# Optimization experiments

Hardware: AMD Instinct MI355X
Metric: run time of the kernel (lower is better)

The kernel has to match this reference:

```python
import jax, jax.numpy as jnp
import numpy as np

B, T = 8, 1024
IN_FEAT = 1024
N_FEAT = 1024
N_HEAD = 16
D_K = N_FEAT // N_HEAD
KERNEL = 11
LEFT_PAD = (KERNEL - 1) // 2  # sanm_shift=0
RIGHT_PAD = KERNEL - 1 - LEFT_PAD


def setup_inputs() -> dict:
    key = jax.random.key(0)
    ks = jax.random.split(key, 7)
    hidden_states = jax.random.normal(ks[0], (B, T, IN_FEAT), dtype=jnp.float32)
    mask = jax.random.randint(ks[1], (B, 1, T), 0, 2, dtype=jnp.int32)
    s_qkv = 1.0 / np.sqrt(IN_FEAT)
    s_out = 1.0 / np.sqrt(N_FEAT)
    W_qkv = jax.random.normal(ks[2], (3 * N_FEAT, IN_FEAT), dtype=jnp.float32) * s_qkv
    b_qkv = jnp.zeros((3 * N_FEAT,), dtype=jnp.float32)
    W_out = jax.random.normal(ks[3], (N_FEAT, N_FEAT), dtype=jnp.float32) * s_out
    b_out = jnp.zeros((N_FEAT,), dtype=jnp.float32)
    fsmn_kernel = jax.random.normal(ks[4], (N_FEAT, 1, KERNEL), dtype=jnp.float32) * (1.0 / KERNEL)
    return {"hidden_states": hidden_states, "mask": mask, "W_qkv": W_qkv,
            "b_qkv": b_qkv, "W_out": W_out, "b_out": b_out, "fsmn_kernel": fsmn_kernel}


def _fsmn(v, maskf, fsmn_kernel):
    # v: [B,T,D], maskf: [B,T,1]
    vm = v * maskf
    x = jnp.transpose(vm, (0, 2, 1))  # [B,D,T]
    x = jnp.pad(x, ((0, 0), (0, 0), (LEFT_PAD, RIGHT_PAD)))
    # depthwise conv1d (cross-correlation, matching torch Conv1d)
    y = jax.lax.conv_general_dilated(
        x, fsmn_kernel, window_strides=(1,), padding='VALID',
        dimension_numbers=('NCH', 'OIH', 'NCH'), feature_group_count=N_FEAT)
    y = jnp.transpose(y, (0, 2, 1)) + vm  # [B,T,D]
    return y * maskf


def reference(hidden_states, mask, W_qkv, b_qkv, W_out, b_out, fsmn_kernel):
    b, t, _ = hidden_states.shape
    qkv = jnp.einsum('btf,of->bto', hidden_states, W_qkv) + b_qkv  # [B,T,3*N_FEAT]
    q, k, v = jnp.split(qkv, 3, axis=-1)
    def heads(x):
        return jnp.transpose(x.reshape(b, t, N_HEAD, D_K), (0, 2, 1, 3))  # [B,H,T,D_K]
    q_h, k_h, v_h = heads(q), heads(k), heads(v)

    maskf = mask.reshape(b, t, 1).astype(hidden_states.dtype)
    fsmn_memory = _fsmn(v, maskf, fsmn_kernel)

    scale = D_K ** -0.5
    scores = jnp.einsum('bhqd,bhkd->bhqk', q_h * scale, k_h)  # [B,H,T,T]
    mask_keys = (mask.reshape(b, 1, 1, t) == 0)  # True where padded
    scores = jnp.where(mask_keys, -jnp.inf, scores)
    attn = jax.nn.softmax(scores, axis=-1)
    attn = jnp.where(mask_keys, 0.0, attn)
    ctx = jnp.einsum('bhqk,bhkd->bhqd', attn, v_h)  # [B,H,T,D_K]
    ctx = jnp.transpose(ctx, (0, 2, 1, 3)).reshape(b, t, N_FEAT)
    att_outs = jnp.einsum('btf,of->bto', ctx, W_out) + b_out
    return att_outs + fsmn_memory
```

## Files before the change

### kernel.cpp

```cpp
#include <hip/hip_runtime.h>
#include <stdint.h>


typedef uint16_t u16;
typedef float f32x4 __attribute__((ext_vector_type(4)));
typedef __bf16 bf16x8 __attribute__((ext_vector_type(8)));
typedef __bf16 bf16x2 __attribute__((ext_vector_type(2)));
typedef u16 u16x8 __attribute__((ext_vector_type(8)));
typedef u16 u16x4 __attribute__((ext_vector_type(4)));
typedef short s16x4 __attribute__((ext_vector_type(4)));

__device__ __forceinline__ u16 f2bf(float f) {
    union { float f; uint32_t u; } c; c.f = f;
    uint32_t u = c.u;
    return (u16)((u + 0x7fffu + ((u >> 16) & 1u)) >> 16);
}
__device__ __forceinline__ float bf2f(u16 h) {
    union { uint32_t u; float f; } c; c.u = ((uint32_t)h) << 16;
    return c.f;
}
__device__ __forceinline__ uint32_t pack_bf16(float a, float b) {
    bf16x2 t; t[0] = (__bf16)a; t[1] = (__bf16)b;
    union { bf16x2 v; uint32_t u; } c; c.v = t; return c.u;
}

__global__ __launch_bounds__(256) void cvt_f32_bf16(const float* __restrict__ src,
                                                    u16* __restrict__ dst, int n) {
    int i = (blockIdx.x * 256 + threadIdx.x) * 4;
    if (i >= n) return;
    float4 v = *reinterpret_cast<const float4*>(src + i);
    ushort4 o;
    o.x = f2bf(v.x); o.y = f2bf(v.y); o.z = f2bf(v.z); o.w = f2bf(v.w);
    *reinterpret_cast<ushort4*>(dst + i) = o;
}

__global__ void maskbits_kernel(const int* __restrict__ mask, uint32_t* __restrict__ mb) {
    int i = threadIdx.x;
    int b = i >> 5, c = i & 31;
    uint32_t u = 0;
    for (int j = 0; j < 32; ++j)
        u |= (mask[(b << 10) + c * 32 + j] ? 1u : 0u) << j;
    mb[i] = u;
}

__global__ __launch_bounds__(256) void fsmn_kt(const float* __restrict__ fk,
                                               float* __restrict__ kt) {
    int idx = blockIdx.x * 256 + threadIdx.x;
    if (idx < 11 * 1024) {
        int j = idx >> 10, c = idx & 1023;
        kt[idx] = fk[c * 11 + j];
    }
}

__global__ __launch_bounds__(256) void transpose_v(const u16* __restrict__ vn,
                                                   u16* __restrict__ vt) {
    __shared__ u16 ts[64][68];
    const int tid = threadIdx.x;
    const int bh = blockIdx.x >> 4;
    const int kc = blockIdx.x & 15;
    const u16* src = vn + ((size_t)bh << 16) + (size_t)kc * 64 * 64;
#pragma unroll
    for (int it = 0; it < 2; ++it) {
        int ch = it * 256 + tid;
        int k = ch >> 3, g = ch & 7;
        *reinterpret_cast<u16x8*>(&ts[k][g * 8]) =
            *reinterpret_cast<const u16x8*>(src + k * 64 + g * 8);
    }
    __syncthreads();
    u16* dst = vt + ((size_t)bh << 16) + kc * 64;
#pragma unroll
    for (int it = 0; it < 2; ++it) {
        int ch = it * 256 + tid;
        int d = ch >> 3, gk = ch & 7;
        u16x8 v;
#pragma unroll
        for (int j = 0; j < 8; ++j) v[j] = ts[gk * 8 + j][d];
        *reinterpret_cast<u16x8*>(dst + (size_t)d * 1024 + gk * 8) = v;
    }
}

template<int MODE>
__global__ __launch_bounds__(512, 4) void gemm_bk32(
    const u16* __restrict__ A, const u16* __restrict__ Bw, int M, int N, int K,
    int ntiles_n, const float* __restrict__ bias,
    u16* __restrict__ qo, u16* __restrict__ ko, u16* __restrict__ vo,
    float* __restrict__ out)
{
    __shared__ u16 lds[24576];
    const int t = threadIdx.x;
    const int lane = t & 63;
    const int wave = t >> 6;
    const int wr = wave >> 2, wc = wave & 3;
    const int lr = lane & 15, lq = lane >> 4;
    const int r3 = lane >> 2, c4 = lane & 3;
    const int cpx = gridDim.x >> 3;
    const int bid = (blockIdx.x & 7) * cpx + (blockIdx.x >> 3);
    const int m0 = (bid / ntiles_n) * 128;
    const int n0 = (bid % ntiles_n) * 256;
    const int NT = K >> 5;

    const u16* AgW  = A  + (size_t)(m0 + wave * 16 + r3) * K + c4 * 8;
    const u16* BgW0 = Bw + (size_t)(n0 + wave * 16 + r3) * K + c4 * 8;
    const u16* BgW1 = BgW0 + (size_t)128 * K;

    auto stage = [&](int buf, int tile) {
        u16* dA  = lds + buf * 12288 + wave * 512;
        u16* dB0 = lds + buf * 12288 + 4096 + wave * 512;
        u16* dB1 = dB0 + 4096;
        __builtin_amdgcn_global_load_lds(
            (const __attribute__((address_space(1))) void*)(AgW + tile * 32),
            (__attribute__((address_space(3))) void*)dA, 16, 0, 0);
        __builtin_amdgcn_global_load_lds(
            (const __attribute__((address_space(1))) void*)(BgW0 + tile * 32),
            (__attribute__((address_space(3))) void*)dB0, 16, 0, 0);
        __builtin_amdgcn_global_load_lds(
            (const __attribute__((address_space(1))) void*)(BgW1 + tile * 32),
            (__attribute__((address_space(3))) void*)dB1, 16, 0, 0);
    };

    f32x4 acc[4][4];
#pragma unroll
    for (int i = 0; i < 4; ++i)
#pragma unroll
        for (int j = 0; j < 4; ++j) acc[i][j] = (f32x4){0.f, 0.f, 0.f, 0.f};

    stage(0, 0);
    asm volatile("s_waitcnt vmcnt(0)" ::: "memory");
    __builtin_amdgcn_s_barrier();

    for (int T = 0; T < NT; ++T) {
        const int p = T & 1;
        const u16* Ab = lds + p * 12288;
        const u16* Bb = Ab + 4096;
        bf16x8 a[4], bb[4];
#pragma unroll
        for (int mm = 0; mm < 4; ++mm)
            a[mm] = *reinterpret_cast<const bf16x8*>(Ab + (wr * 64 + mm * 16 + lr) * 32 + lq * 8);
#pragma unroll
        for (int nn = 0; nn < 4; ++nn)
            bb[nn] = *reinterpret_cast<const bf16x8*>(Bb + (wc * 64 + nn * 16 + lr) * 32 + lq * 8);
        if (T + 1 < NT) stage(p ^ 1, T + 1);
        __builtin_amdgcn_s_setprio(1);
#pragma unroll
        for (int mm = 0; mm < 4; ++mm)
#pragma unroll
            for (int nn = 0; nn < 4; ++nn)
                acc[mm][nn] = __builtin_amdgcn_mfma_f32_16x16x32_bf16(a[mm], bb[nn], acc[mm][nn], 0, 0, 0);
        __builtin_amdgcn_s_setprio(0);
        if (T + 1 < NT) asm volatile("s_waitcnt vmcnt(0)" ::: "memory");
        __builtin_amdgcn_s_barrier();
    }

#pragma unroll
    for (int m = 0; m < 4; ++m) {
        int row = m0 + wr * 64 + m * 16 + lq * 4;
#pragma unroll
        for (int n = 0; n < 4; ++n) {
            int col = n0 + wc * 64 + n * 16 + lr;
            float bv = bias[col];
#pragma unroll
            for (int r = 0; r < 4; ++r) {
                float val = acc[m][n][r] + bv;
                int rr = row + r;
                if (MODE == 0) {
                    int part = col >> 10;
                    int cc = col & 1023;
                    int h = cc >> 6, d = cc & 63;
                    int b = rr >> 10, tt = rr & 1023;
                    size_t bh = (size_t)(b * 16 + h);
                    u16* dst = (part == 0) ? qo : (part == 1) ? ko : vo;
                    dst[((bh << 10) + tt) * 64 + d] = f2bf(part == 0 ? val * 0.18033688011f : val);
                } else {
                    size_t o = (size_t)rr * N + col;
                    out[o] += val;
                }
            }
        }
    }
}

__global__ __launch_bounds__(256) void fsmn_v3(const u16* __restrict__ vt,
                                               const int* __restrict__ mask,
                                               const float* __restrict__ kt,
                                               float* __restrict__ out)
{
    __shared__ float vs[64][147];
    __shared__ float ms[144];
    const int tid = threadIdx.x;
    const int tc = blockIdx.x & 7;
    const int bh = blockIdx.x >> 3;
    const int b = bh >> 4, h = bh & 15;
    const int t0 = tc * 128;
    const u16* vrow = vt + ((size_t)bh << 16);
    const int* mrow = mask + (b << 10);

    if (tid < 144) {
        int tt = t0 - 8 + tid;
        ms[tid] = (tt >= 0 && tt < 1024) ? (float)mrow[tt] : 0.f;
    }
    const int sd = tid >> 2;
    const int ci0 = tid & 3;
#pragma unroll
    for (int it = 0; it < 5; ++it) {
        int ci = ci0 + it * 4;
        if (ci < 18) {
            int tbase = t0 - 8 + ci * 8;
            if (tbase >= 0 && tbase < 1024) {
                u16x8 v8 = *reinterpret_cast<const u16x8*>(vrow + (size_t)sd * 1024 + tbase);
#pragma unroll
                for (int j = 0; j < 8; ++j)
                    vs[sd][ci * 8 + j] = bf2f((u16)v8[j]) * (float)mrow[tbase + j];
            } else {
#pragma unroll
                for (int j = 0; j < 8; ++j) vs[sd][ci * 8 + j] = 0.f;
            }
        }
    }
    __syncthreads();

    const int dd = tid & 63;
    const int tg = tid >> 6;
    const int c = h * 64 + dd;
    float kc[11];
#pragma unroll
    for (int j = 0; j < 11; ++j) kc[j] = kt[j * 1024 + c];

    const int tl0 = tg * 32;
    float w[11];
#pragma unroll
    for (int j = 0; j < 11; ++j) w[j] = vs[dd][3 + tl0 + j];
    float* orow = out + ((size_t)(b * 1024 + t0 + tl0)) * 1024 + c;
#pragma unroll 4
    for (int s = 0; s < 32; ++s) {
        float acc = 0.f;
#pragma unroll
        for (int j = 0; j < 11; ++j) acc += kc[j] * w[j];
        float mf = ms[8 + tl0 + s];
        orow[(size_t)s * 1024] = (acc + w[5]) * mf;
#pragma unroll
        for (int j = 0; j < 10; ++j) w[j] = w[j + 1];
        w[10] = vs[dd][3 + tl0 + s + 11];
    }
}

__global__ __launch_bounds__(512) void attn_v9(const u16* __restrict__ qg,
                                               const u16* __restrict__ kg,
                                               const u16* __restrict__ vtg,
                                               const uint32_t* __restrict__ mbits,
                                               u16* __restrict__ ctx)
{
    __shared__ u16 K_s[2][64 * 64];
    __shared__ u16 V_s[2][64 * 64];
    const int t = threadIdx.x;
    const int lane = t & 63;
    const int w = t >> 6;
    const int lr = lane & 15, lq = lane >> 4;
    const int bh = blockIdx.x & 127;
    const int qc = blockIdx.x >> 7;
    const int b = bh >> 4, h = bh & 15;
    const size_t base = (size_t)bh << 16;
    const u16* kb = kg + base;
    const u16* vb = vtg + base;
    const int q0 = qc * 256 + w * 32;

    bf16x8 qf[2][2];
#pragma unroll
    for (int qt = 0; qt < 2; ++qt)
#pragma unroll
        for (int kk = 0; kk < 2; ++kk)
            qf[qt][kk] = *reinterpret_cast<const bf16x8*>(
                qg + base + (size_t)(q0 + qt * 16 + lr) * 64 + kk * 32 + lq * 8);

    f32x4 oacc[2][4];
    f32x4 oacc_l[2];
#pragma unroll
    for (int qt = 0; qt < 2; ++qt) {
        oacc_l[qt] = (f32x4){0.f, 0.f, 0.f, 0.f};
#pragma unroll
        for (int dt = 0; dt < 4; ++dt) oacc[qt][dt] = (f32x4){0.f, 0.f, 0.f, 0.f};
    }

    s16x4 ones_f;
#pragma unroll
    for (int j = 0; j < 4; ++j) ones_f[j] = (short)0x3F80;

    const uint32_t* mrow = mbits + b * 32;

    auto stage = [&](int bufi, int tile) {
        const int k0s = tile * 64;
        int ch = w * 64 + lane;
        int row = ch >> 3, c7 = ch & 7;
        int sc = (c7 ^ (row & 7)) * 8;
        const u16* srcK = kb + (size_t)(k0s + row) * 64 + sc;
        const u16* srcV = vb + (size_t)row * 1024 + k0s + sc;
        u16* dK = &K_s[bufi][(size_t)(w * 64) * 8];
        u16* dV = &V_s[bufi][(size_t)(w * 64) * 8];
        __builtin_amdgcn_global_load_lds(
            (const __attribute__((address_space(1))) void*)srcK,
            (__attribute__((address_space(3))) void*)dK, 16, 0, 0);
        __builtin_amdgcn_global_load_lds(
            (const __attribute__((address_space(1))) void*)srcV,
            (__attribute__((address_space(3))) void*)dV, 16, 0, 0);
    };

    int cur = 0;
    stage(0, 0);
    asm volatile("s_waitcnt vmcnt(0)");
    __syncthreads();

    for (int it = 0; it < 16; ++it) {
        if (it < 15) stage(cur ^ 1, it + 1);

        const u16* Kb = K_s[cur];
        bf16x8 kf[4][2];
#pragma unroll
        for (int kt = 0; kt < 4; ++kt) {
            int row = kt * 16 + lr;
#pragma unroll
            for (int kk = 0; kk < 2; ++kk) {
                int g = (kk * 4 + lq) ^ (row & 7);
                kf[kt][kk] = *reinterpret_cast<const bf16x8*>(Kb + row * 64 + g * 8);
            }
        }

        const uint32_t mw0 = mrow[it * 2], mw1 = mrow[it * 2 + 1];
        uint32_t mb_[4];
        mb_[0] = mw0 >> (lq * 4);
        mb_[1] = mw0 >> (16 + lq * 4);
        mb_[2] = mw1 >> (lq * 4);
        mb_[3] = mw1 >> (16 + lq * 4);
        f32x4 ma[4];
#pragma unroll
        for (int kt = 0; kt < 4; ++kt)
#pragma unroll
            for (int r = 0; r < 4; ++r)
                ma[kt][r] = (mb_[kt] & (1u << r)) ? 0.f : -3e38f;

        const u16* Vb = V_s[cur];
        s16x4 vf[4][4];
#pragma unroll
        for (int ks = 0; ks < 4; ++ks)
#pragma unroll
            for (int dt = 0; dt < 4; ++dt) {
                int row = dt * 16 + lr;
                int g = (ks * 2 + (lq >> 1)) ^ (row & 7);
                vf[ks][dt] = *reinterpret_cast<const s16x4*>(Vb + row * 64 + g * 8 + (lq & 1) * 4);
            }

#pragma unroll
        for (int qt = 0; qt < 2; ++qt) {
            f32x4 s[4];
            __builtin_amdgcn_s_setprio(1);
#pragma unroll
            for (int kt = 0; kt < 4; ++kt) {
                s[kt] = __builtin_amdgcn_mfma_f32_16x16x32_bf16(kf[kt][0], qf[qt][0], ma[kt], 0, 0, 0);
                s[kt] = __builtin_amdgcn_mfma_f32_16x16x32_bf16(kf[kt][1], qf[qt][1], s[kt], 0, 0, 0);
            }
            __builtin_amdgcn_s_setprio(0);

            union { uint32_t u[2]; s16x4 v; } pa[4];
#pragma unroll
            for (int kt = 0; kt < 4; ++kt) {
                float p0 = __builtin_amdgcn_exp2f(s[kt][0]);
                float p1 = __builtin_amdgcn_exp2f(s[kt][1]);
                float p2 = __builtin_amdgcn_exp2f(s[kt][2]);
                float p3 = __builtin_amdgcn_exp2f(s[kt][3]);
                pa[kt].u[0] = pack_bf16(p0, p1);
                pa[kt].u[1] = pack_bf16(p2, p3);
            }

            __builtin_amdgcn_s_setprio(1);
#pragma unroll
            for (int dt = 0; dt < 4; ++dt) {
                f32x4 o = oacc[qt][dt];
#pragma unroll
                for (int kt = 0; kt < 4; ++kt)
                    o = __builtin_amdgcn_mfma_f32_16x16x16bf16_1k(vf[kt][dt], pa[kt].v, o, 0, 0, 0);
                oacc[qt][dt] = o;
            }
#pragma unroll
            for (int kt = 0; kt < 4; ++kt)
                oacc_l[qt] = __builtin_amdgcn_mfma_f32_16x16x16bf16_1k(ones_f, pa[kt].v, oacc_l[qt], 0, 0, 0);
            __builtin_amdgcn_s_setprio(0);
        }

        asm volatile("s_waitcnt vmcnt(0)" ::: "memory");
        __syncthreads();
        cur ^= 1;
    }

#pragma unroll
    for (int qt = 0; qt < 2; ++qt) {
        float li = 1.f / oacc_l[qt][0];
        int trow = q0 + qt * 16 + lr;
        u16* crow = ctx + ((size_t)(b << 10) + trow) * 1024 + h * 64;
#pragma unroll
        for (int dt = 0; dt < 4; ++dt) {
            f32x4 o = oacc[qt][dt];
            u16x4 pkv;
            pkv[0] = f2bf(o[0] * li); pkv[1] = f2bf(o[1] * li);
            pkv[2] = f2bf(o[2] * li); pkv[3] = f2bf(o[3] * li);
            *reinterpret_cast<u16x4*>(crow + dt * 16 + lq * 4) = pkv;
        }
    }
}

extern "C" void kernel_launch(void* const* d_in, const int* in_sizes, int n_in,
                              void* d_out, int out_size, void* d_ws, size_t ws_size,
                              hipStream_t stream)
{
    (void)in_sizes; (void)n_in; (void)out_size; (void)ws_size;
    const float* hs   = (const float*)d_in[0];
    const int*   mask = (const int*)d_in[1];
    const float* Wqkv = (const float*)d_in[2];
    const float* bqkv = (const float*)d_in[3];
    const float* Wout = (const float*)d_in[4];
    const float* bout = (const float*)d_in[5];
    const float* fk   = (const float*)d_in[6];
    float* out = (float*)d_out;

    char* ws = (char*)d_ws;
    u16* hsb   = (u16*)(ws);
    u16* wqkvb = (u16*)(ws + 16777216);
    u16* woutb = (u16*)(ws + 23068672);
    u16* qb    = (u16*)(ws + 25165824);
    u16* kb    = (u16*)(ws + 41943040);
    u16* vtb   = (u16*)(ws + 58720256);
    u16* vnb   = (u16*)(ws + 75497472);
    u16* ctxb  = (u16*)(ws + 75497472);
    uint32_t* mbits = (uint32_t*)ws;
    float* ktT = (float*)(ws + 4096);

    cvt_f32_bf16<<<8192, 256, 0, stream>>>(hs,   hsb,   8388608);
    cvt_f32_bf16<<<3072, 256, 0, stream>>>(Wqkv, wqkvb, 3145728);
    cvt_f32_bf16<<<1024, 256, 0, stream>>>(Wout, woutb, 1048576);

    gemm_bk32<0><<<64 * 12, 512, 0, stream>>>(hsb, wqkvb, 8192, 3072, 1024, 12,
                                              bqkv, qb, kb, vnb, nullptr);
    maskbits_kernel<<<1, 256, 0, stream>>>(mask, mbits);
    fsmn_kt<<<44, 256, 0, stream>>>(fk, ktT);
    transpose_v<<<2048, 256, 0, stream>>>(vnb, vtb);
    fsmn_v3<<<1024, 256, 0, stream>>>(vtb, mask, ktT, out);
    attn_v9<<<512, 512, 0, stream>>>(qb, kb, vtb, mbits, ctxb);
    gemm_bk32<1><<<64 * 4, 512, 0, stream>>>(ctxb, woutb, 8192, 1024, 1024, 4,
                                             bout, nullptr, nullptr, nullptr, out);
}
```

Measured before the change: 207.0 us.

## Triple-buffer GEMM LDS pipeline and merge small preprocessing kernels

The GEMM mainloop moves from double to triple buffering in LDS. It prefetches two K-tiles ahead and waits on vmcnt(3) instead of draining all loads each iteration, so global-to-LDS latency is better hidden. The three f32-to-bf16 conversion launches are merged into one, and the maskbits and fsmn kernel-transpose launches are merged into another, to cut launch overhead. The catch is LDS use: it rises from 48KB to 72KB per block, which may reduce occupancy below the 4 blocks per CU that launch_bounds requests.

```diff
diff --git a/kernel.cpp b/kernel.cpp
--- a/kernel.cpp
+++ b/kernel.cpp
@@ -24,31 +24,38 @@
     union { bf16x2 v; uint32_t u; } c; c.v = t; return c.u;
 }
 
-__global__ __launch_bounds__(256) void cvt_f32_bf16(const float* __restrict__ src,
-                                                    u16* __restrict__ dst, int n) {
-    int i = (blockIdx.x * 256 + threadIdx.x) * 4;
-    if (i >= n) return;
+__global__ __launch_bounds__(256) void cvt_all(const float* __restrict__ hs,
+                                               const float* __restrict__ wqkv,
+                                               const float* __restrict__ wout,
+                                               u16* __restrict__ hsb,
+                                               u16* __restrict__ wqkvb,
+                                               u16* __restrict__ woutb) {
+    int bid = blockIdx.x;
+    const float* src; u16* dst; int ib;
+    if (bid < 8192)       { src = hs;   dst = hsb;   ib = bid; }
+    else if (bid < 11264) { src = wqkv; dst = wqkvb; ib = bid - 8192; }
+    else                  { src = wout; dst = woutb; ib = bid - 11264; }
+    int i = (ib * 256 + threadIdx.x) * 4;
     float4 v = *reinterpret_cast<const float4*>(src + i);
     ushort4 o;
     o.x = f2bf(v.x); o.y = f2bf(v.y); o.z = f2bf(v.z); o.w = f2bf(v.w);
     *reinterpret_cast<ushort4*>(dst + i) = o;
 }
 
-__global__ void maskbits_kernel(const int* __restrict__ mask, uint32_t* __restrict__ mb) {
-    int i = threadIdx.x;
-    int b = i >> 5, c = i & 31;
-    uint32_t u = 0;
-    for (int j = 0; j < 32; ++j)
-        u |= (mask[(b << 10) + c * 32 + j] ? 1u : 0u) << j;
-    mb[i] = u;
-}
-
-__global__ __launch_bounds__(256) void fsmn_kt(const float* __restrict__ fk,
-                                               float* __restrict__ kt) {
-    int idx = blockIdx.x * 256 + threadIdx.x;
-    if (idx < 11 * 1024) {
+__global__ void mask_and_kt(const int* __restrict__ mask, uint32_t* __restrict__ mb,
+                            const float* __restrict__ fk, float* __restrict__ kt) {
+    int bid = blockIdx.x;
+    if (bid < 44) {
+        int idx = bid * 256 + threadIdx.x;
         int j = idx >> 10, c = idx & 1023;
         kt[idx] = fk[c * 11 + j];
+    } else {
+        int i = threadIdx.x;
+        int b = i >> 5, c = i & 31;
+        uint32_t u = 0;
+        for (int j = 0; j < 32; ++j)
+            u |= (mask[(b << 10) + c * 32 + j] ? 1u : 0u) << j;
+        mb[i] = u;
     }
 }
 
@@ -86,7 +93,7 @@
     u16* __restrict__ qo, u16* __restrict__ ko, u16* __restrict__ vo,
     float* __restrict__ out)
 {
-    __shared__ u16 lds[24576];
+    __shared__ u16 lds[36864];
     const int t = threadIdx.x;
     const int lane = t & 63;
     const int wave = t >> 6;
@@ -125,12 +132,13 @@
         for (int j = 0; j < 4; ++j) acc[i][j] = (f32x4){0.f, 0.f, 0.f, 0.f};
 
     stage(0, 0);
-    asm volatile("s_waitcnt vmcnt(0)" ::: "memory");
+    stage(1, 1);
+    asm volatile("s_waitcnt vmcnt(3)" ::: "memory");
     __builtin_amdgcn_s_barrier();
 
     for (int T = 0; T < NT; ++T) {
-        const int p = T & 1;
-        const u16* Ab = lds + p * 12288;
+        const int bcur = T % 3;
+        const u16* Ab = lds + bcur * 12288;
         const u16* Bb = Ab + 4096;
         bf16x8 a[4], bb[4];
 #pragma unroll
@@ -139,7 +147,7 @@
 #pragma unroll
         for (int nn = 0; nn < 4; ++nn)
             bb[nn] = *reinterpret_cast<const bf16x8*>(Bb + (wc * 64 + nn * 16 + lr) * 32 + lq * 8);
-        if (T + 1 < NT) stage(p ^ 1, T + 1);
+        if (T + 2 < NT) stage((T + 2) % 3, T + 2);
         __builtin_amdgcn_s_setprio(1);
 #pragma unroll
         for (int mm = 0; mm < 4; ++mm)
@@ -147,8 +155,9 @@
             for (int nn = 0; nn < 4; ++nn)
                 acc[mm][nn] = __builtin_amdgcn_mfma_f32_16x16x32_bf16(a[mm], bb[nn], acc[mm][nn], 0, 0, 0);
         __builtin_amdgcn_s_setprio(0);
-        if (T + 1 < NT) asm volatile("s_waitcnt vmcnt(0)" ::: "memory");
-        __builtin_amdgcn_s_barrier();
+        if (T + 2 < NT)      asm volatile("s_waitcnt vmcnt(3)" ::: "memory");
+        else if (T + 1 < NT) asm volatile("s_waitcnt vmcnt(0)" ::: "memory");
+        if (T + 1 < NT) __builtin_amdgcn_s_barrier();
     }
 
 #pragma unroll
@@ -431,14 +440,11 @@
     uint32_t* mbits = (uint32_t*)ws;
     float* ktT = (float*)(ws + 4096);
 
-    cvt_f32_bf16<<<8192, 256, 0, stream>>>(hs,   hsb,   8388608);
-    cvt_f32_bf16<<<3072, 256, 0, stream>>>(Wqkv, wqkvb, 3145728);
-    cvt_f32_bf16<<<1024, 256, 0, stream>>>(Wout, woutb, 1048576);
+    cvt_all<<<12288, 256, 0, stream>>>(hs, Wqkv, Wout, hsb, wqkvb, woutb);
 
     gemm_bk32<0><<<64 * 12, 512, 0, stream>>>(hsb, wqkvb, 8192, 3072, 1024, 12,
                                               bqkv, qb, kb, vnb, nullptr);
-    maskbits_kernel<<<1, 256, 0, stream>>>(mask, mbits);
-    fsmn_kt<<<44, 256, 0, stream>>>(fk, ktT);
+    mask_and_kt<<<45, 256, 0, stream>>>(mask, mbits, fk, ktT);
     transpose_v<<<2048, 256, 0, stream>>>(vnb, vtb);
     fsmn_v3<<<1024, 256, 0, stream>>>(vtb, mask, ktT, out);
     attn_v9<<<512, 512, 0, stream>>>(qb, kb, vtb, mbits, ctxb);
```

Measured after the change: 197.8 us. 1.05x faster.
